# Optimization experiments

Measured on AMD Instinct MI355X. Metric: run time of the kernel, lower is better.

Reference implementation:

```python
import jax, jax.numpy as jnp
import numpy as np

B, N, F, H, M, EF, OUT = 256, 32, 40, 100, 100, 4, 128
MESSAGE_PASSES = 3


def setup_inputs() -> dict:
    key = jax.random.key(0)
    ks = jax.random.split(key, 8)
    # Deterministic ring graphs: node i <-> node (i+1)%N, one-hot bond type.
    # Every node has degree 2 -> static nonzero counts.
    rng = np.random.default_rng(0)
    edges = np.zeros((B, N, N, EF), np.float32)
    b = np.arange(B)[:, None]
    i = np.arange(N)[None, :]
    j = (i + 1) % N
    t = rng.integers(0, EF, size=(B, N))
    edges[b, i, j, t] = 1.0
    edges[b, j, i, t] = 1.0

    nodes = jax.random.normal(ks[0], (B, N, F), jnp.float32)

    def init(k, shape, fan):
        return jax.random.normal(k, shape, jnp.float32) / np.sqrt(fan).astype(np.float32)

    W_msg = init(ks[1], (M, H, EF), H)          # MNN edge-conditioned weights
    W_ih = init(ks[2], (3 * H, M), M)            # GRUCell input weights
    W_hh = init(ks[3], (3 * H, H), H)            # GRUCell hidden weights
    b_ih = jnp.zeros((3 * H,), jnp.float32)
    b_hh = jnp.zeros((3 * H,), jnp.float32)
    Wg = init(ks[4], (H + F, H), H + F)          # gather gate
    bg = jnp.zeros((H,), jnp.float32)
    We = init(ks[5], (H, H), H)                  # gather embed
    be = jnp.zeros((H,), jnp.float32)
    Wo = init(ks[6], (H, OUT), H)                # output head
    bo = jnp.zeros((OUT,), jnp.float32)

    return {
        "nodes": nodes, "edges": jnp.asarray(edges),
        "W_msg": W_msg, "W_ih": W_ih, "W_hh": W_hh, "b_ih": b_ih, "b_hh": b_hh,
        "Wg": Wg, "bg": bg, "We": We, "be": be, "Wo": Wo, "bo": bo,
        "n_edges": B * N * 2, "n_node_entries": B * N,
    }


def gru_cell(x, h, W_ih, W_hh, b_ih, b_hh):
    gi = x @ W_ih.T + b_ih
    gh = h @ W_hh.T + b_hh
    ir, iz, inn = jnp.split(gi, 3, axis=-1)
    hr, hz, hn = jnp.split(gh, 3, axis=-1)
    r = jax.nn.sigmoid(ir + hr)
    z = jax.nn.sigmoid(iz + hz)
    n = jnp.tanh(inn + r * hn)
    return (1.0 - z) * n + z * h


def reference(nodes, edges, W_msg, W_ih, W_hh, b_ih, b_hh, Wg, bg, We, be, Wo, bo,
              n_edges, n_node_entries):
    adjacency = jnp.sum(edges, axis=3)                      # (B, N, N)
    eb, en, eg = jnp.nonzero(adjacency, size=n_edges)       # edge-level indices
    nb, nn_ = jnp.nonzero(adjacency.sum(-1), size=n_node_entries)

    # Dense one-hot segment-sum matrix: (n_node_entries, n_edges)
    same = (nb[:, None] == eb) & (nn_[:, None] == en)
    msg_sum_mat = same.astype(jnp.float32)

    edge_batch_edges = edges[eb, en, eg, :]                 # (E, EF)

    hidden = jnp.zeros((B, N, H), jnp.float32).at[:, :, :F].set(nodes)
    node_h = hidden[nb, nn_, :]                             # (V, H)

    for _ in range(MESSAGE_PASSES):
        nghb_h = hidden[eb, eg, :]                          # (E, H)
        # MNN message: sum_f edges[e,f] * W_msg[m,h,f] * nghb[e,h]
        message_terms = jnp.einsum('ef,mhf,eh->em', edge_batch_edges, W_msg, nghb_h)
        messages = msg_sum_mat @ message_terms              # (V, M) dense one-hot matmul
        node_h = gru_cell(messages, node_h, W_ih, W_hh, b_ih, b_hh)
        hidden = hidden.at[nb, nn_, :].set(node_h)

    node_mask = (adjacency.sum(-1) != 0).astype(jnp.float32)  # (B, N)
    cat = jnp.concatenate([hidden, nodes], axis=-1)           # (B, N, H+F)
    gate = jax.nn.sigmoid(cat @ Wg + bg)
    emb = gate * (hidden @ We + be)
    graph_emb = jnp.sum(emb * node_mask[..., None], axis=1)   # (B, H)
    return graph_emb @ Wo + bo                                # (B, OUT)
```

## Files before the change

kernel.cpp:

```cpp
#include <hip/hip_runtime.h>
#include <cstddef>
#include <cstdint>

#define B_   256
#define N_   32
#define F_   40
#define H_   100
#define OUT_ 128
#define CAP_ 8
#define TB   1024
#define XCS  168
#define XMS  136
#define NBLK 343
#define NLO  63

using bf16x8 = __attribute__((ext_vector_type(8))) short;
using f32x4  = __attribute__((ext_vector_type(4))) float;

#define MFMA(a,b,c) __builtin_amdgcn_mfma_f32_16x16x32_bf16((a),(b),(c),0,0,0)

__device__ __forceinline__ float sigmoidf_(float x){ return 1.0f/(1.0f+__expf(-x)); }
__device__ __forceinline__ float tanhf_(float x){
  float e = __expf(2.0f*x);
  return 1.0f - 2.0f/(e+1.0f);
}
__device__ __forceinline__ float bf2f(short s){ return __uint_as_float(((uint32_t)(uint16_t)s)<<16); }
__device__ __forceinline__ short f2bf(float x){
  uint32_t u = __float_as_uint(x);
  return (short)((u + 0x7FFFu + ((u>>16)&1u))>>16);
}
__device__ __forceinline__ void bsplit(float x, short& hi, short& lo){
  hi = f2bf(x);
  lo = f2bf(x - bf2f(hi));
}

__global__ void prep_frags4(const float* __restrict__ Wmsg,
                            const float* __restrict__ Wih,
                            const float* __restrict__ Whh,
                            const float* __restrict__ Wg,
                            const float* __restrict__ We,
                            short* __restrict__ AFhi,
                            short* __restrict__ AFlo){
  int slot = blockIdx.x*blockDim.x + threadIdx.x;
  if (slot >= NBLK*512) return;
  int blk = slot>>9, r = slot&511, lane = r>>3, jj = r&7;
  int m = lane&15, q = lane>>4, kl = q*8+jj;
  float v = 0.0f;
  if (blk < 112){
    int t = blk/28, rem = blk%28, jmt = rem>>2, ks = rem&3;
    int mg = jmt*16+m, h = ks*32+kl;
    if (mg<100 && h<100) v = Wmsg[(mg*100+h)*4 + t];
    AFhi[slot] = f2bf(v);
  } else if (blk < 280){
    int bb = blk-112, mat = bb/28, rem = bb%28, jmt = rem>>2, ks = rem&3;
    int mg = jmt*16+m, k = ks*32+kl;
    if (mg<100 && k<100)
      v = (mat<3) ? Wih[(mat*100+mg)*100+k] : Whh[((mat-3)*100+mg)*100+k];
    AFhi[slot] = f2bf(v);
  } else if (blk < 315){
    int bb = blk-280, jmt = bb/5, ks = bb%5;
    int mg = jmt*16+m, k = ks*32+kl;
    if (mg<100 && k<140) v = Wg[k*100+mg];
    short hi,lo; bsplit(v,hi,lo);
    AFhi[slot] = hi;
    AFlo[(size_t)(blk-280)*512 + r] = lo;
  } else {
    int bb = blk-315, jmt = bb>>2, ks = bb&3;
    int mg = jmt*16+m, k = ks*32+kl;
    if (mg<100 && k<100) v = We[k*100+mg];
    short hi,lo; bsplit(v,hi,lo);
    AFhi[slot] = hi;
    AFlo[(size_t)(blk-280)*512 + r] = lo;
  }
}

__global__ __launch_bounds__(TB, 4) void mpnn_mfma(
    const float* __restrict__ nodes, const float* __restrict__ edges,
    const short* __restrict__ AFhi, const short* __restrict__ AFlo,
    const float* __restrict__ b_ih, const float* __restrict__ b_hh,
    const float* __restrict__ bg, const float* __restrict__ be,
    const float* __restrict__ Wo, const float* __restrict__ bo,
    float* __restrict__ out){
  const int b = blockIdx.x;
  const int tid = threadIdx.x;
  const int lane = tid & 63;
  const int w = tid >> 6;

  __shared__ short XcH[32*XCS], XcL[32*XCS];
  __shared__ short XmH[32*XMS];
  __shared__ short XyH[4][32*XMS];
  __shared__ float sh_ge[H_];
  __shared__ float sh_part[4][OUT_];
  __shared__ float sh_rowsum[N_];
  __shared__ int   sh_cnt[N_];
  __shared__ int   sh_gt[N_][CAP_];
  __shared__ float sh_w[N_][CAP_];

  for (int i=tid;i<(32*XCS)/2;i+=TB){ ((int*)XcH)[i]=0; ((int*)XcL)[i]=0; }
  for (int i=tid;i<(32*XMS)/2;i+=TB){ ((int*)XmH)[i]=0; }
  if (tid < H_) sh_ge[tid]=0.0f;
  if (tid < N_){ sh_cnt[tid]=0; sh_rowsum[tid]=0.0f; }
  __syncthreads();

  {
    int n = tid>>5, g = tid&31;
    const float4 ev = *(const float4*)(edges + (((size_t)b*N_+n)*N_+g)*4);
    float adj = ev.x+ev.y+ev.z+ev.w;
    if (adj != 0.0f){
      atomicAdd(&sh_rowsum[n], adj);
      float ef[4] = {ev.x,ev.y,ev.z,ev.w};
      for (int f=0; f<4; ++f)
        if (ef[f] != 0.0f){
          int s = atomicAdd(&sh_cnt[n],1);
          if (s<CAP_){ sh_gt[n][s]=(g<<2)|f; sh_w[n][s]=ef[f]; }
        }
    }
  }
  for (int p=tid; p<N_*F_; p+=TB){
    int n = p/F_, f = p%F_;
    float x = nodes[((size_t)b*N_+n)*F_ + f];
    short hi,lo; bsplit(x,hi,lo);
    XcH[n*XCS+f]=hi;      XcL[n*XCS+f]=lo;
    XcH[n*XCS+100+f]=hi;
  }
  __syncthreads();

  const int jmt = w>>1, nt = w&1;
  const bool task = (w < 14);
  const int nrow = nt*16 + (lane&15);
  const int boff = (lane>>4)*8;

  for (int pass=0; pass<3; ++pass){
    for (int it=0; it<2; ++it){
      int idx = tid + it*TB;
      int n = idx >> 6;
      int kp = idx & 63;
      int cnt = sh_cnt[n] < CAP_ ? sh_cnt[n] : CAP_;
      float s0[4]={0,0,0,0}, s1[4]={0,0,0,0};
      for (int e=0;e<cnt;++e){
        int gt = sh_gt[n][e];
        int g = gt>>2; float wv = sh_w[n][e];
        int hh = ((const int*)(XcH + g*XCS))[kp];
        float h0 = bf2f((short)(hh&0xffff));
        float h1 = bf2f((short)(hh>>16));
        int t = gt&3;
        if (t==0)      { s0[0]+=wv*h0; s1[0]+=wv*h1; }
        else if (t==1) { s0[1]+=wv*h0; s1[1]+=wv*h1; }
        else if (t==2) { s0[2]+=wv*h0; s1[2]+=wv*h1; }
        else           { s0[3]+=wv*h0; s1[3]+=wv*h1; }
      }
#pragma unroll
      for (int t=0;t<4;++t){
        ((int*)(XyH[t] + n*XMS))[kp] =
          (int)((uint16_t)f2bf(s0[t]) | ((uint32_t)(uint16_t)f2bf(s1[t])<<16));
      }
    }
    __syncthreads();
    f32x4 Ch0=(f32x4)0.0f, Ch1=(f32x4)0.0f, Ch2=(f32x4)0.0f;
    if (task){
      f32x4 Cm=(f32x4)0.0f;
#pragma unroll 1
      for (int t=0;t<4;++t){
        const short* pa = AFhi + ((size_t)(t*28 + jmt*4))*512 + lane*8;
        const short* pb = XyH[t] + nrow*XMS + boff;
        bf16x8 a0 = *(const bf16x8*)(pa);
        bf16x8 a1 = *(const bf16x8*)(pa+512);
        bf16x8 a2 = *(const bf16x8*)(pa+1024);
        bf16x8 a3 = *(const bf16x8*)(pa+1536);
        bf16x8 b0 = *(const bf16x8*)(pb);
        bf16x8 b1 = *(const bf16x8*)(pb+32);
        bf16x8 b2 = *(const bf16x8*)(pb+64);
        bf16x8 b3 = *(const bf16x8*)(pb+96);
        Cm = MFMA(a0,b0,Cm); Cm = MFMA(a1,b1,Cm);
        Cm = MFMA(a2,b2,Cm); Cm = MFMA(a3,b3,Cm);
      }
      {
        const short* pb = XcH + nrow*XCS + boff;
        bf16x8 b0 = *(const bf16x8*)(pb);
        bf16x8 b1 = *(const bf16x8*)(pb+32);
        bf16x8 b2 = *(const bf16x8*)(pb+64);
        bf16x8 b3 = *(const bf16x8*)(pb+96);
        const short* pa = AFhi + ((size_t)(112 + 3*28 + jmt*4))*512 + lane*8;
        {
          bf16x8 a0=*(const bf16x8*)(pa),      a1=*(const bf16x8*)(pa+512);
          bf16x8 a2=*(const bf16x8*)(pa+1024), a3=*(const bf16x8*)(pa+1536);
          Ch0 = MFMA(a0,b0,Ch0); Ch0 = MFMA(a1,b1,Ch0);
          Ch0 = MFMA(a2,b2,Ch0); Ch0 = MFMA(a3,b3,Ch0);
        }
        pa += 28*512;
        {
          bf16x8 a0=*(const bf16x8*)(pa),      a1=*(const bf16x8*)(pa+512);
          bf16x8 a2=*(const bf16x8*)(pa+1024), a3=*(const bf16x8*)(pa+1536);
          Ch1 = MFMA(a0,b0,Ch1); Ch1 = MFMA(a1,b1,Ch1);
          Ch1 = MFMA(a2,b2,Ch1); Ch1 = MFMA(a3,b3,Ch1);
        }
        pa += 28*512;
        {
          bf16x8 a0=*(const bf16x8*)(pa),      a1=*(const bf16x8*)(pa+512);
          bf16x8 a2=*(const bf16x8*)(pa+1024), a3=*(const bf16x8*)(pa+1536);
          Ch2 = MFMA(a0,b0,Ch2); Ch2 = MFMA(a1,b1,Ch2);
          Ch2 = MFMA(a2,b2,Ch2); Ch2 = MFMA(a3,b3,Ch2);
        }
      }
      for (int r=0;r<4;++r){
        int row = jmt*16 + (lane>>4)*4 + r;
        if (row<100) XmH[nrow*XMS+row] = f2bf(Cm[r]);
      }
    }
    __syncthreads();
    if (task){
      f32x4 Ci0=(f32x4)0.0f, Ci1=(f32x4)0.0f, Ci2=(f32x4)0.0f;
      {
        const short* pb = XmH + nrow*XMS + boff;
        bf16x8 b0 = *(const bf16x8*)(pb);
        bf16x8 b1 = *(const bf16x8*)(pb+32);
        bf16x8 b2 = *(const bf16x8*)(pb+64);
        bf16x8 b3 = *(const bf16x8*)(pb+96);
        const short* pa = AFhi + ((size_t)(112 + jmt*4))*512 + lane*8;
        {
          bf16x8 a0=*(const bf16x8*)(pa),      a1=*(const bf16x8*)(pa+512);
          bf16x8 a2=*(const bf16x8*)(pa+1024), a3=*(const bf16x8*)(pa+1536);
          Ci0 = MFMA(a0,b0,Ci0); Ci0 = MFMA(a1,b1,Ci0);
          Ci0 = MFMA(a2,b2,Ci0); Ci0 = MFMA(a3,b3,Ci0);
        }
        pa += 28*512;
        {
          bf16x8 a0=*(const bf16x8*)(pa),      a1=*(const bf16x8*)(pa+512);
          bf16x8 a2=*(const bf16x8*)(pa+1024), a3=*(const bf16x8*)(pa+1536);
          Ci1 = MFMA(a0,b0,Ci1); Ci1 = MFMA(a1,b1,Ci1);
          Ci1 = MFMA(a2,b2,Ci1); Ci1 = MFMA(a3,b3,Ci1);
        }
        pa += 28*512;
        {
          bf16x8 a0=*(const bf16x8*)(pa),      a1=*(const bf16x8*)(pa+512);
          bf16x8 a2=*(const bf16x8*)(pa+1024), a3=*(const bf16x8*)(pa+1536);
          Ci2 = MFMA(a0,b0,Ci2); Ci2 = MFMA(a1,b1,Ci2);
          Ci2 = MFMA(a2,b2,Ci2); Ci2 = MFMA(a3,b3,Ci2);
        }
      }
      bool msk = (sh_rowsum[nrow] != 0.0f);
#pragma unroll
      for (int r=0;r<4;++r){
        int row = jmt*16 + (lane>>4)*4 + r;
        if (row<100){
          float ho = bf2f(XcH[nrow*XCS+row]) + bf2f(XcL[nrow*XCS+row]);
          float rr = sigmoidf_(Ci0[r]+Ch0[r] + b_ih[row]     + b_hh[row]);
          float zz = sigmoidf_(Ci1[r]+Ch1[r] + b_ih[100+row] + b_hh[100+row]);
          float nn = tanhf_(Ci2[r] + b_ih[200+row] + rr*(Ch2[r] + b_hh[200+row]));
          float hnew = (1.0f-zz)*nn + zz*ho;
          if (!msk) hnew = ho;
          short hi,lo; bsplit(hnew,hi,lo);
          XcH[nrow*XCS+row]=hi; XcL[nrow*XCS+row]=lo;
        }
      }
    }
    __syncthreads();
  }

  f32x4 Cg=(f32x4)0.0f, Ce=(f32x4)0.0f;
  if (task){
    const short* pb = XcH + nrow*XCS + boff;
    bf16x8 b0 = *(const bf16x8*)(pb);
    bf16x8 b1 = *(const bf16x8*)(pb+32);
    bf16x8 b2 = *(const bf16x8*)(pb+64);
    bf16x8 b3 = *(const bf16x8*)(pb+96);
    bf16x8 b4 = *(const bf16x8*)(pb+128);
    {
      const short* ph = AFhi + ((size_t)(280 + jmt*5))*512 + lane*8;
      const short* pl = AFlo + ((size_t)(jmt*5))*512 + lane*8;
      Cg = MFMA(*(const bf16x8*)(ph),      b0, Cg);
      Cg = MFMA(*(const bf16x8*)(pl),      b0, Cg);
      Cg = MFMA(*(const bf16x8*)(ph+512),  b1, Cg);
      Cg = MFMA(*(const bf16x8*)(pl+512),  b1, Cg);
      Cg = MFMA(*(const bf16x8*)(ph+1024), b2, Cg);
      Cg = MFMA(*(const bf16x8*)(pl+1024), b2, Cg);
      Cg = MFMA(*(const bf16x8*)(ph+1536), b3, Cg);
      Cg = MFMA(*(const bf16x8*)(pl+1536), b3, Cg);
      Cg = MFMA(*(const bf16x8*)(ph+2048), b4, Cg);
      Cg = MFMA(*(const bf16x8*)(pl+2048), b4, Cg);
    }
    {
      const short* ph = AFhi + ((size_t)(315 + jmt*4))*512 + lane*8;
      const short* pl = AFlo + ((size_t)(35 + jmt*4))*512 + lane*8;
      Ce = MFMA(*(const bf16x8*)(ph),      b0, Ce);
      Ce = MFMA(*(const bf16x8*)(pl),      b0, Ce);
      Ce = MFMA(*(const bf16x8*)(ph+512),  b1, Ce);
      Ce = MFMA(*(const bf16x8*)(pl+512),  b1, Ce);
      Ce = MFMA(*(const bf16x8*)(ph+1024), b2, Ce);
      Ce = MFMA(*(const bf16x8*)(pl+1024), b2, Ce);
      Ce = MFMA(*(const bf16x8*)(ph+1536), b3, Ce);
      Ce = MFMA(*(const bf16x8*)(pl+1536), b3, Ce);
    }
    bool msk = (sh_rowsum[nrow] != 0.0f);
#pragma unroll
    for (int r=0;r<4;++r){
      int row = jmt*16 + (lane>>4)*4 + r;
      float v = 0.0f;
      if (row<100){
        float gate = sigmoidf_(Cg[r] + bg[row]);
        float emb  = gate*(Ce[r] + be[row]);
        v = msk ? emb : 0.0f;
      }
      v += __shfl_xor(v, 1);
      v += __shfl_xor(v, 2);
      v += __shfl_xor(v, 4);
      v += __shfl_xor(v, 8);
      if (row<100 && (lane&15)==0) atomicAdd(&sh_ge[row], v);
    }
  }
  __syncthreads();
  if (tid < 512){
    int o = tid & 127, q = tid >> 7;
    float s = 0.0f;
    int k0 = 25*q;
#pragma unroll 5
    for (int k=k0; k<k0+25; ++k) s += sh_ge[k]*Wo[k*OUT_+o];
    sh_part[q][o] = s;
  }
  __syncthreads();
  if (tid < OUT_){
    out[(size_t)b*OUT_ + tid] = bo[tid] + sh_part[0][tid] + sh_part[1][tid]
                              + sh_part[2][tid] + sh_part[3][tid];
  }
}

extern "C" void kernel_launch(void* const* d_in, const int* in_sizes, int n_in,
                              void* d_out, int out_size, void* d_ws, size_t ws_size,
                              hipStream_t stream){
  const float* nodes = (const float*)d_in[0];
  const float* edges = (const float*)d_in[1];
  const float* W_msg = (const float*)d_in[2];
  const float* W_ih  = (const float*)d_in[3];
  const float* W_hh  = (const float*)d_in[4];
  const float* b_ih  = (const float*)d_in[5];
  const float* b_hh  = (const float*)d_in[6];
  const float* Wg    = (const float*)d_in[7];
  const float* bg    = (const float*)d_in[8];
  const float* We    = (const float*)d_in[9];
  const float* be    = (const float*)d_in[10];
  const float* Wo    = (const float*)d_in[11];
  const float* bo    = (const float*)d_in[12];

  short* AFhi = (short*)d_ws;
  short* AFlo = AFhi + (size_t)NBLK*512;

  prep_frags4<<<(NBLK*512 + 255)/256, 256, 0, stream>>>(W_msg, W_ih, W_hh, Wg, We,
                                                        AFhi, AFlo);
  mpnn_mfma<<<B_, TB, 0, stream>>>(nodes, edges, AFhi, AFlo, b_ih, b_hh, bg, be,
                                   Wo, bo, (float*)d_out);
}
```

Before: 117.4 us.

## Replace sparse neighbor gather with dense MFMA adjacency matmul per edge type

```diff
diff --git a/kernel.cpp b/kernel.cpp
--- a/kernel.cpp
+++ b/kernel.cpp
@@ -7,10 +7,10 @@
 #define F_   40
 #define H_   100
 #define OUT_ 128
-#define CAP_ 8
 #define TB   1024
 #define XCS  168
 #define XMS  136
+#define ST2  40
 #define NBLK 343
 #define NLO  63
 
@@ -87,34 +87,31 @@
   const int w = tid >> 6;
 
   __shared__ short XcH[32*XCS], XcL[32*XCS];
+  __shared__ short XcT[112*ST2];
   __shared__ short XmH[32*XMS];
   __shared__ short XyH[4][32*XMS];
+  __shared__ short Aw[4][32*32];
   __shared__ float sh_ge[H_];
   __shared__ float sh_part[4][OUT_];
   __shared__ float sh_rowsum[N_];
-  __shared__ int   sh_cnt[N_];
-  __shared__ int   sh_gt[N_][CAP_];
-  __shared__ float sh_w[N_][CAP_];
 
   for (int i=tid;i<(32*XCS)/2;i+=TB){ ((int*)XcH)[i]=0; ((int*)XcL)[i]=0; }
   for (int i=tid;i<(32*XMS)/2;i+=TB){ ((int*)XmH)[i]=0; }
+  for (int i=tid;i<(112*ST2)/2;i+=TB){ ((int*)XcT)[i]=0; }
+  for (int i=tid;i<(4*32*XMS)/2;i+=TB){ ((int*)XyH)[i]=0; }
   if (tid < H_) sh_ge[tid]=0.0f;
-  if (tid < N_){ sh_cnt[tid]=0; sh_rowsum[tid]=0.0f; }
+  if (tid < N_) sh_rowsum[tid]=0.0f;
   __syncthreads();
 
   {
     int n = tid>>5, g = tid&31;
     const float4 ev = *(const float4*)(edges + (((size_t)b*N_+n)*N_+g)*4);
     float adj = ev.x+ev.y+ev.z+ev.w;
-    if (adj != 0.0f){
-      atomicAdd(&sh_rowsum[n], adj);
-      float ef[4] = {ev.x,ev.y,ev.z,ev.w};
-      for (int f=0; f<4; ++f)
-        if (ef[f] != 0.0f){
-          int s = atomicAdd(&sh_cnt[n],1);
-          if (s<CAP_){ sh_gt[n][s]=(g<<2)|f; sh_w[n][s]=ef[f]; }
-        }
-    }
+    if (adj != 0.0f) atomicAdd(&sh_rowsum[n], adj);
+    Aw[0][n*32+g] = f2bf(ev.x);
+    Aw[1][n*32+g] = f2bf(ev.y);
+    Aw[2][n*32+g] = f2bf(ev.z);
+    Aw[3][n*32+g] = f2bf(ev.w);
   }
   for (int p=tid; p<N_*F_; p+=TB){
     int n = p/F_, f = p%F_;
@@ -122,6 +119,7 @@
     short hi,lo; bsplit(x,hi,lo);
     XcH[n*XCS+f]=hi;      XcL[n*XCS+f]=lo;
     XcH[n*XCS+100+f]=hi;
+    XcT[f*ST2+n]=hi;
   }
   __syncthreads();
 
@@ -131,28 +129,18 @@
   const int boff = (lane>>4)*8;
 
   for (int pass=0; pass<3; ++pass){
-    for (int it=0; it<2; ++it){
-      int idx = tid + it*TB;
-      int n = idx >> 6;
-      int kp = idx & 63;
-      int cnt = sh_cnt[n] < CAP_ ? sh_cnt[n] : CAP_;
-      float s0[4]={0,0,0,0}, s1[4]={0,0,0,0};
-      for (int e=0;e<cnt;++e){
-        int gt = sh_gt[n][e];
-        int g = gt>>2; float wv = sh_w[n][e];
-        int hh = ((const int*)(XcH + g*XCS))[kp];
-        float h0 = bf2f((short)(hh&0xffff));
-        float h1 = bf2f((short)(hh>>16));
-        int t = gt&3;
-        if (t==0)      { s0[0]+=wv*h0; s1[0]+=wv*h1; }
-        else if (t==1) { s0[1]+=wv*h0; s1[1]+=wv*h1; }
-        else if (t==2) { s0[2]+=wv*h0; s1[2]+=wv*h1; }
-        else           { s0[3]+=wv*h0; s1[3]+=wv*h1; }
-      }
+    if (task){
+      bf16x8 at = *(const bf16x8*)&XcT[(jmt*16+(lane&15))*ST2 + boff];
+      int kbase = jmt*16 + boff/2;
 #pragma unroll
       for (int t=0;t<4;++t){
-        ((int*)(XyH[t] + n*XMS))[kp] =
-          (int)((uint16_t)f2bf(s0[t]) | ((uint32_t)(uint16_t)f2bf(s1[t])<<16));
+        bf16x8 bt = *(const bf16x8*)&Aw[t][nrow*32 + boff];
+        f32x4 D = (f32x4)0.0f;
+        D = MFMA(at, bt, D);
+        short4 pk;
+        pk.x = f2bf(D[0]); pk.y = f2bf(D[1]);
+        pk.z = f2bf(D[2]); pk.w = f2bf(D[3]);
+        *(short4*)&XyH[t][nrow*XMS + kbase] = pk;
       }
     }
     __syncthreads();
@@ -251,6 +239,7 @@
           if (!msk) hnew = ho;
           short hi,lo; bsplit(hnew,hi,lo);
           XcH[nrow*XCS+row]=hi; XcL[nrow*XCS+row]=lo;
+          XcT[row*ST2+nrow]=hi;
         }
       }
     }
```

Measured after the change: 114.5 us. -2.4%, faster.
